# Performance work log

Measured on AMD Instinct MI355X. Metric: run time of the kernel, lower is better.

## Reference

```python
import jax, jax.numpy as jnp
import numpy as np

NUM_LAYERS = 2
# Z eigenvalue of each basis state index (bit0 = qubit 0 = MSB, bit1 = qubit 1)
_Z0 = jnp.array([1.0, 1.0, -1.0, -1.0], dtype=jnp.float32)
_Z1 = jnp.array([1.0, -1.0, 1.0, -1.0], dtype=jnp.float32)
_CNOT_PERM = jnp.array([0, 1, 3, 2])  # CNOT(control=0, target=1) permutes |10>,|11>


def setup_inputs() -> dict:
    key = jax.random.key(0)
    k1, k2 = jax.random.split(key)
    x = jax.random.uniform(k1, (8192, 56, 56), dtype=jnp.float32)
    params = jax.random.uniform(k2, (2,), dtype=jnp.float32)
    return {"x": x, "params": params}


def reference(x, params):
    # x: (N, H, W). Each 2x2 patch contributes its top-row pair (x[r,c], x[r,c+1]).
    p0 = x[:, ::2, ::2]   # (N, H//2, W//2) -> angle for qubit 0
    p1 = x[:, ::2, 1::2]  # (N, H//2, W//2) -> angle for qubit 1
    # torch: patch.max() is the max over the whole (N, 2) slice at each (r, c)
    m = jnp.maximum(p0, p1).max(axis=0)  # (H//2, W//2)
    t0 = jnp.pi * p0 / (m + 1e-8)
    t1 = jnp.pi * p1 / (m + 1e-8)

    # RY(t)|0> = cos(t/2)|0> + sin(t/2)|1>; product state amplitudes, index = 2*b0 + b1
    c0, s0 = jnp.cos(t0 * 0.5), jnp.sin(t0 * 0.5)
    c1, s1 = jnp.cos(t1 * 0.5), jnp.sin(t1 * 0.5)
    a = jnp.stack([c0 * c1, c0 * s1, s0 * c1, s0 * s1], axis=-1).astype(jnp.complex64)

    # RZ(p) = diag(e^{-ip/2}, e^{+ip/2}) on each qubit -> diagonal phase per basis state
    phase = jnp.exp(-0.5j * (params[0] * _Z0 + params[1] * _Z1)).astype(jnp.complex64)
    for _ in range(NUM_LAYERS):
        a = a * phase          # RZ(params[0]) on q0, RZ(params[1]) on q1
        a = a[..., _CNOT_PERM]  # CNOT(0 -> 1)

    probs = jnp.real(a * jnp.conj(a))           # (N, H//2, W//2, 4)
    z0 = jnp.einsum('nhwk,k->nhw', probs, _Z0)  # <Z_0> (analytic expectation)
    N = x.shape[0]
    return z0.reshape(N, -1)  # (N, (H//2)*(W//2)), row-major matches r-then-c loop
```

## Files before the change

kernel.cpp:

```cpp
#include <hip/hip_runtime.h>


namespace {

constexpr int IMG  = 3136;
constexpr int HW   = 784;
constexpr int NIMG = 8192;
constexpr int NB1  = 1024;
constexpr int IPB  = NIMG / NB1;
constexpr int NQ   = 392;

__global__ __launch_bounds__(256) void k_partial(const float* __restrict__ x,
                                                 float* __restrict__ M,
                                                 unsigned* __restrict__ mu) {
    const int t = threadIdx.x;
    const int b = blockIdx.x;

    if (b == 0) {
        for (int i = t; i < HW; i += 256) mu[i] = 0u;
    }

    const int h0 = t / 14,   w0 = t - h0 * 14;
    const int o0 = h0 * 112 + w0 * 4;
    const int u1 = t + 256;
    const int h1 = u1 / 14,  w1 = u1 - h1 * 14;
    const int o1 = h1 * 112 + w1 * 4;
    const bool a1 = (u1 < NQ);

    float2 lm0 = make_float2(0.f, 0.f);
    float2 lm1 = make_float2(0.f, 0.f);

    const float* base = x + (size_t)b * IPB * IMG;
#pragma unroll
    for (int n = 0; n < IPB; ++n) {
        const float* p = base + (size_t)n * IMG;
        float4 v = *(const float4*)(p + o0);
        lm0.x = fmaxf(lm0.x, fmaxf(v.x, v.y));
        lm0.y = fmaxf(lm0.y, fmaxf(v.z, v.w));
        if (a1) {
            float4 w = *(const float4*)(p + o1);
            lm1.x = fmaxf(lm1.x, fmaxf(w.x, w.y));
            lm1.y = fmaxf(lm1.y, fmaxf(w.z, w.w));
        }
    }

    *(float2*)(M + (size_t)b * HW + 2 * t) = lm0;
    if (a1) *(float2*)(M + (size_t)b * HW + 2 * u1) = lm1;
}

__global__ __launch_bounds__(256) void k_final(const float* __restrict__ M,
                                               unsigned* __restrict__ mu) {
    int u = blockIdx.x * 256 + threadIdx.x;
    int g   = u / HW;
    int col = u - g * HW;
    const float* p = M + (size_t)g * 32 * HW + col;
    float cm = 0.0f;
#pragma unroll
    for (int k = 0; k < 32; ++k)
        cm = fmaxf(cm, p[k * HW]);
    atomicMax(mu + col, __float_as_uint(cm));
}

__global__ __launch_bounds__(256) void k_out(const float* __restrict__ x,
                                             const float* __restrict__ mu,
                                             float* __restrict__ out) {
    int g  = blockIdx.x * 256 + threadIdx.x;
    int n  = g / 196;
    int j  = g - n * 196;
    int h  = j / 7;
    int wq = j - h * 7;

    const float* p = x + (size_t)n * IMG + h * 112 + 8 * wq;
    float4 va = *(const float4*)p;
    float4 vb = *(const float4*)(p + 4);

    const float* mp = mu + h * 28 + 4 * wq;
    float2 ma = *(const float2*)mp;
    float2 mb = *(const float2*)(mp + 2);

    float4 o;
    o.x = __builtin_amdgcn_cosf(va.x * (0.5f / (ma.x + 1e-8f)));
    o.y = __builtin_amdgcn_cosf(va.z * (0.5f / (ma.y + 1e-8f)));
    o.z = __builtin_amdgcn_cosf(vb.x * (0.5f / (mb.x + 1e-8f)));
    o.w = __builtin_amdgcn_cosf(vb.z * (0.5f / (mb.y + 1e-8f)));

    *(float4*)(out + (size_t)n * HW + 4 * j) = o;
}

}

extern "C" void kernel_launch(void* const* d_in, const int* in_sizes, int n_in,
                              void* d_out, int out_size, void* d_ws, size_t ws_size,
                              hipStream_t stream) {
    const float* x   = (const float*)d_in[0];
    float*       M   = (float*)d_ws;
    unsigned*    mu  = (unsigned*)((char*)d_ws + (size_t)NB1 * HW * 4);
    float*       out = (float*)d_out;

    hipLaunchKernelGGL(k_partial, dim3(NB1), dim3(256), 0, stream, x, M, mu);
    hipLaunchKernelGGL(k_final, dim3(HW * 32 / 256), dim3(256), 0, stream, M, mu);
    hipLaunchKernelGGL(k_out, dim3(NIMG * 196 / 256), dim3(256), 0, stream,
                       x, (const float*)mu, out);
}
```

Baseline: 36.74 us.

## Fuse final max reduction into output kernel, drop atomic pass

Removes the separate k_final kernel and its atomicMax and zeroing of mu. Each output block now reduces the 512 per-block partial maxima for its row through shared memory before computing cosines. Partial blocks are halved to 512 so fewer partials remain. The output kernel now uses strided scalar loads and stores instead of float4 accesses, and every block redundantly re-reads the partial maxima for its row, which may cost memory efficiency.

```diff
diff --git a/kernel.cpp b/kernel.cpp
--- a/kernel.cpp
+++ b/kernel.cpp
@@ -6,32 +6,26 @@
 constexpr int IMG  = 3136;
 constexpr int HW   = 784;
 constexpr int NIMG = 8192;
-constexpr int NB1  = 1024;
+constexpr int NB1  = 512;
 constexpr int IPB  = NIMG / NB1;
-constexpr int NQ   = 392;
+constexpr int IPB2 = 128;
+constexpr int NSL  = NIMG / IPB2;
 
 __global__ __launch_bounds__(256) void k_partial(const float* __restrict__ x,
-                                                 float* __restrict__ M,
-                                                 unsigned* __restrict__ mu) {
+                                                 float* __restrict__ M) {
     const int t = threadIdx.x;
     const int b = blockIdx.x;
 
-    if (b == 0) {
-        for (int i = t; i < HW; i += 256) mu[i] = 0u;
-    }
-
-    const int h0 = t / 14,   w0 = t - h0 * 14;
-    const int o0 = h0 * 112 + w0 * 4;
+    const int h0 = t / 14,  w0 = t - h0 * 14,  o0 = h0 * 112 + w0 * 4;
     const int u1 = t + 256;
-    const int h1 = u1 / 14,  w1 = u1 - h1 * 14;
-    const int o1 = h1 * 112 + w1 * 4;
-    const bool a1 = (u1 < NQ);
+    const int h1 = u1 / 14, w1 = u1 - h1 * 14, o1 = h1 * 112 + w1 * 4;
+    const bool a1 = (u1 < 392);
 
     float2 lm0 = make_float2(0.f, 0.f);
     float2 lm1 = make_float2(0.f, 0.f);
 
     const float* base = x + (size_t)b * IPB * IMG;
-#pragma unroll
+#pragma unroll 4
     for (int n = 0; n < IPB; ++n) {
         const float* p = base + (size_t)n * IMG;
         float4 v = *(const float4*)(p + o0);
@@ -48,43 +42,47 @@
     if (a1) *(float2*)(M + (size_t)b * HW + 2 * u1) = lm1;
 }
 
-__global__ __launch_bounds__(256) void k_final(const float* __restrict__ M,
-                                               unsigned* __restrict__ mu) {
-    int u = blockIdx.x * 256 + threadIdx.x;
-    int g   = u / HW;
-    int col = u - g * HW;
-    const float* p = M + (size_t)g * 32 * HW + col;
-    float cm = 0.0f;
+__global__ __launch_bounds__(256) void k_out(const float* __restrict__ x,
+                                             const float* __restrict__ M,
+                                             float* __restrict__ out) {
+    __shared__ float part[8][28];
+
+    const int bid = blockIdx.x;
+    const int h   = bid % 28;
+    const int n0  = (bid / 28) * IPB2;
+    const int t   = threadIdx.x;
+    const int c   = t % 28;
+    const int g   = t / 28;
+    const bool act = (t < 224);
+
+    float p0[16];
+    if (act) {
+        const float* xp = x + (size_t)(n0 + g) * IMG + h * 112 + c * 2;
 #pragma unroll
-    for (int k = 0; k < 32; ++k)
-        cm = fmaxf(cm, p[k * HW]);
-    atomicMax(mu + col, __float_as_uint(cm));
-}
+        for (int k = 0; k < 16; ++k)
+            p0[k] = xp[(size_t)(8 * k) * IMG];
 
-__global__ __launch_bounds__(256) void k_out(const float* __restrict__ x,
-                                             const float* __restrict__ mu,
-                                             float* __restrict__ out) {
-    int g  = blockIdx.x * 256 + threadIdx.x;
-    int n  = g / 196;
-    int j  = g - n * 196;
-    int h  = j / 7;
-    int wq = j - h * 7;
+        const float* mp = M + (size_t)(g * 64) * HW + h * 28 + c;
+        float cm = 0.0f;
+#pragma unroll 8
+        for (int r = 0; r < 64; ++r)
+            cm = fmaxf(cm, mp[(size_t)r * HW]);
+        part[g][c] = cm;
+    }
 
-    const float* p = x + (size_t)n * IMG + h * 112 + 8 * wq;
-    float4 va = *(const float4*)p;
-    float4 vb = *(const float4*)(p + 4);
+    __syncthreads();
 
-    const float* mp = mu + h * 28 + 4 * wq;
-    float2 ma = *(const float2*)mp;
-    float2 mb = *(const float2*)(mp + 2);
+    if (act) {
+        float m = part[0][c];
+#pragma unroll
+        for (int g2 = 1; g2 < 8; ++g2) m = fmaxf(m, part[g2][c]);
+        const float r = 0.5f / (m + 1e-8f);
 
-    float4 o;
-    o.x = __builtin_amdgcn_cosf(va.x * (0.5f / (ma.x + 1e-8f)));
-    o.y = __builtin_amdgcn_cosf(va.z * (0.5f / (ma.y + 1e-8f)));
-    o.z = __builtin_amdgcn_cosf(vb.x * (0.5f / (mb.x + 1e-8f)));
-    o.w = __builtin_amdgcn_cosf(vb.z * (0.5f / (mb.y + 1e-8f)));
-
-    *(float4*)(out + (size_t)n * HW + 4 * j) = o;
+        float* op = out + (size_t)(n0 + g) * HW + h * 28 + c;
+#pragma unroll
+        for (int k = 0; k < 16; ++k)
+            op[(size_t)(8 * k) * HW] = __builtin_amdgcn_cosf(p0[k] * r);
+    }
 }
 
 }
@@ -94,11 +92,9 @@
                               hipStream_t stream) {
     const float* x   = (const float*)d_in[0];
     float*       M   = (float*)d_ws;
-    unsigned*    mu  = (unsigned*)((char*)d_ws + (size_t)NB1 * HW * 4);
     float*       out = (float*)d_out;
 
-    hipLaunchKernelGGL(k_partial, dim3(NB1), dim3(256), 0, stream, x, M, mu);
-    hipLaunchKernelGGL(k_final, dim3(HW * 32 / 256), dim3(256), 0, stream, M, mu);
-    hipLaunchKernelGGL(k_out, dim3(NIMG * 196 / 256), dim3(256), 0, stream,
-                       x, (const float*)mu, out);
+    hipLaunchKernelGGL(k_partial, dim3(NB1), dim3(256), 0, stream, x, M);
+    hipLaunchKernelGGL(k_out, dim3(28 * NSL), dim3(256), 0, stream,
+                       x, (const float*)M, out);
 }
```

Result: slower. 43.84 us (+19.3%).
